# Kernel optimization log

Hardware: AMD Instinct MI355X
Metric: run time of the kernel (lower is better)

## Reference

```python
import jax, jax.numpy as jnp
import numpy as np

# dims
T, B = 64, 512
NTOK, NINP, NHID = 512, 600, 600
NB, TOPK = 6, 4          # num_blocks, update_topk
BS = NHID // NB          # block_size = 100
ATT, DK, DC = 340, 64, 32  # attention_out, input-attn key dim, comm-attn key dim


def setup_inputs() -> dict:
    key = jax.random.key(0)
    ks = jax.random.split(key, 16)
    s = 0.05
    r = lambda k, shp: (jax.random.normal(k, shp, jnp.float32) * s)
    return {
        "input": jax.random.normal(ks[0], (T, B, NTOK), jnp.float32),
        "hidden": jnp.zeros((1, B, NHID), jnp.float32),
        "masks": jnp.ones((T, B, 1), jnp.float32),
        "enc_W": r(ks[1], (NTOK, NINP)),
        "enc_b": jnp.zeros((NINP,), jnp.float32),
        "Wq": r(ks[2], (BS, DK)),
        "Wk": r(ks[3], (NINP, DK)),
        "Wv": r(ks[4], (NINP, ATT)),
        "Wx": r(ks[5], (ATT, 3 * BS)),
        "Wh": r(ks[6], (BS, 3 * BS)),
        "gru_b": jnp.zeros((3 * BS,), jnp.float32),
        "Wq2": r(ks[7], (BS, DC)),
        "Wk2": r(ks[8], (BS, DC)),
        "Wv2": r(ks[9], (BS, BS)),
        "dec_W": r(ks[10], (NHID, NTOK)),
        "dec_b": jnp.zeros((NTOK,), jnp.float32),
    }


def reference(input, hidden, masks, enc_W, enc_b, Wq, Wk, Wv, Wx, Wh, gru_b,
              Wq2, Wk2, Wv2, dec_W, dec_b):
    # encoder (continuous input path of RNNModel)
    emb = input @ enc_W + enc_b                     # [T,B,ninp]
    h0 = hidden[0]                                  # [B,nhid]
    sc1 = 1.0 / jnp.sqrt(jnp.float32(DK))
    sc2 = 1.0 / jnp.sqrt(jnp.float32(DC))

    def step(h, xt_m):
        xt, m = xt_m                                # [B,ninp], [B,1]
        h = h * m                                   # RL done-masking (h_masks)
        hb = h.reshape(B, NB, BS)                   # per-block hidden
        # --- input attention: read sources = [null, input] (num_modules_read_input=2)
        src = jnp.stack([jnp.zeros_like(xt), xt], axis=1)   # [B,2,ninp]
        kk = src @ Wk                               # [B,2,DK]
        vv = src @ Wv                               # [B,2,ATT]
        q = hb @ Wq                                 # [B,NB,DK]
        probs = jax.nn.softmax(jnp.einsum('bnd,bsd->bns', q, kk) * sc1, axis=-1)
        read = jnp.einsum('bns,bsv->bnv', probs, vv)        # [B,NB,ATT]
        # --- top-k block selection: blocks attending most to real input update
        inp_score = probs[:, :, 1]                  # [B,NB]
        _, idx = jax.lax.top_k(inp_score, TOPK)
        bmask = jax.nn.one_hot(idx, NB, dtype=h.dtype).sum(axis=1)  # [B,NB]
        # --- shared block GRU update
        xg = read @ Wx + gru_b                      # [B,NB,3*BS]
        hg = hb @ Wh                                # [B,NB,3*BS]
        r_ = jax.nn.sigmoid(xg[..., :BS] + hg[..., :BS])
        z_ = jax.nn.sigmoid(xg[..., BS:2 * BS] + hg[..., BS:2 * BS])
        n_ = jnp.tanh(xg[..., 2 * BS:] + r_ * hg[..., 2 * BS:])
        hn = (1.0 - z_) * n_ + z_ * hb              # [B,NB,BS]
        # --- communication attention among blocks (residual)
        q2, k2, v2 = hn @ Wq2, hn @ Wk2, hn @ Wv2
        p2 = jax.nn.softmax(jnp.einsum('bnd,bmd->bnm', q2, k2) * sc2, axis=-1)
        hc = hn + jnp.einsum('bnm,bmv->bnv', p2, v2)
        # --- gated write: only top-k blocks update
        mb = bmask[..., None]
        hb_new = mb * hc + (1.0 - mb) * hb
        hnew = hb_new.reshape(B, NHID)
        return hnew, (hnew, bmask)

    hT, (out, bmasks) = jax.lax.scan(step, h0, (emb, masks))
    dec = out @ dec_W + dec_b                       # [T,B,ntoken]
    return dec, hT[None], bmasks
```

## Files before the change

kernel.cpp:

```cpp
#include <hip/hip_runtime.h>
#include <hip/hip_bf16.h>
#include <stdint.h>

typedef __bf16 bf16_t;
typedef __bf16 bf16x8 __attribute__((ext_vector_type(8)));
typedef float f32x4 __attribute__((ext_vector_type(4)));

#define T_STEPS 64
#define BATCH   512
#define NTOKC   512
#define NINP    600
#define NHID    600
#define NBLK    6
#define BSZ     100
#define DK      64
#define ATTD    340
#define DC      32
#define KU_N    384
#define OUT_KP  608

#define WS_KU     0u
#define WS_OUTB   50331648u
#define WS_W1     90177536u
#define WS_B1     90963968u
#define WS_WVWX   90965504u
#define WS_DECWT  91685504u


__global__ void prep_wvwx(const float* __restrict__ Wv, const float* __restrict__ Wx,
                          float* __restrict__ WvWx) {
    int idx = blockIdx.x * 256 + threadIdx.x;
    if (idx >= NINP * 300) return;
    int i = idx / 300, c = idx % 300;
    float acc = 0.f;
    for (int a = 0; a < ATTD; a++) acc += Wv[i * ATTD + a] * Wx[a * 300 + c];
    WvWx[i * 300 + c] = acc;
}

__global__ void prep_w1(const float* __restrict__ encW, const float* __restrict__ Wk,
                        const float* __restrict__ WvWx, float* __restrict__ W1) {
    int idx = blockIdx.x * 256 + threadIdx.x;
    if (idx >= NTOKC * KU_N) return;
    int i = idx / KU_N, c = idx % KU_N;
    float acc = 0.f;
    if (c < DK) {
        for (int k = 0; k < NINP; k++) acc += encW[i * NINP + k] * Wk[k * DK + c];
    } else if (c < DK + 300) {
        int cc = c - DK;
        for (int k = 0; k < NINP; k++) acc += encW[i * NINP + k] * WvWx[k * 300 + cc];
    }
    W1[idx] = acc;
}

__global__ void prep_b1(const float* __restrict__ encB, const float* __restrict__ Wk,
                        const float* __restrict__ WvWx, float* __restrict__ b1) {
    int c = blockIdx.x * 256 + threadIdx.x;
    if (c >= KU_N) return;
    float acc = 0.f;
    if (c < DK) {
        for (int k = 0; k < NINP; k++) acc += encB[k] * Wk[k * DK + c];
    } else if (c < DK + 300) {
        int cc = c - DK;
        for (int k = 0; k < NINP; k++) acc += encB[k] * WvWx[k * 300 + cc];
    }
    b1[c] = acc;
}

__global__ void prep_decwt(const float* __restrict__ decW, bf16_t* __restrict__ decWT) {
    int idx = blockIdx.x * 256 + threadIdx.x;
    if (idx >= NTOKC * OUT_KP) return;
    int n = idx / OUT_KP, k = idx % OUT_KP;
    decWT[idx] = (k < NHID) ? (bf16_t)decW[k * NTOKC + n] : (bf16_t)0.f;
}


__global__ __launch_bounds__(256) void ku_gemm(const float* __restrict__ A,
                                               const float* __restrict__ W1,
                                               const float* __restrict__ b1,
                                               float* __restrict__ KU) {
    __shared__ float As[16][128];
    __shared__ float Bs[16][64];
    const int tid = threadIdx.x;
    const int m0 = blockIdx.x * 128, n0 = blockIdx.y * 64;
    const int ty = tid >> 4, tx = tid & 15;
    const int bk = tid >> 6, bn = tid & 63;
    float acc[8][4] = {};
    for (int k0 = 0; k0 < NTOKC; k0 += 16) {
#pragma unroll
        for (int ii = 0; ii < 2; ii++) {
            int t2 = tid + ii * 256;
            int ar = t2 >> 2, ac4 = (t2 & 3) << 2;
            float4 raw = *(const float4*)(A + (size_t)(m0 + ar) * NTOKC + k0 + ac4);
            As[ac4 + 0][ar] = raw.x;
            As[ac4 + 1][ar] = raw.y;
            As[ac4 + 2][ar] = raw.z;
            As[ac4 + 3][ar] = raw.w;
        }
#pragma unroll
        for (int i = 0; i < 4; i++) {
            int kk = bk + (i << 2);
            Bs[kk][bn] = W1[(size_t)(k0 + kk) * KU_N + n0 + bn];
        }
        __syncthreads();
#pragma unroll
        for (int kk = 0; kk < 16; kk++) {
            float4 a0 = *(const float4*)&As[kk][ty * 8];
            float4 a1 = *(const float4*)&As[kk][ty * 8 + 4];
            float4 bv = *(const float4*)&Bs[kk][tx * 4];
            float av[8] = {a0.x, a0.y, a0.z, a0.w, a1.x, a1.y, a1.z, a1.w};
            float bw[4] = {bv.x, bv.y, bv.z, bv.w};
#pragma unroll
            for (int r = 0; r < 8; r++)
#pragma unroll
                for (int c = 0; c < 4; c++) acc[r][c] += av[r] * bw[c];
        }
        __syncthreads();
    }
#pragma unroll
    for (int r = 0; r < 8; r++) {
        int m = m0 + ty * 8 + r;
#pragma unroll
        for (int c = 0; c < 4; c++) {
            int n = n0 + tx * 4 + c;
            KU[(size_t)m * KU_N + n] = acc[r][c] + b1[n];
        }
    }
}


__global__ __launch_bounds__(640) void scan_kernel(
    const float* __restrict__ hidden, const float* __restrict__ masks,
    const float* __restrict__ Wq, const float* __restrict__ Wh,
    const float* __restrict__ grub, const float* __restrict__ Wq2,
    const float* __restrict__ Wk2, const float* __restrict__ Wv2,
    const float* __restrict__ KU, bf16_t* __restrict__ outb,
    float* __restrict__ hT_out, float* __restrict__ bm_out) {
    __shared__ float h[2][NHID];
    __shared__ float u[2][300];
    __shared__ float k1s[2][DK];
    __shared__ float qb[2][NBLK][DK];
    __shared__ float p1s[2][8], bmv[2][8];
    __shared__ float hg[2][NBLK][300];
    __shared__ float qkv[2][NBLK][164];
    __shared__ float p2s[2][NBLK][8];

    const int tid = threadIdx.x;
    const int b0 = blockIdx.x * 2;

    for (int idx = tid; idx < 2 * NHID; idx += 640) {
        int b = idx / NHID, j = idx % NHID;
        h[b][j] = hidden[(size_t)(b0 + b) * NHID + j];
    }
    __syncthreads();

    for (int t = 0; t < T_STEPS; t++) {
        {
            float mv0 = masks[t * BATCH + b0];
            float mv1 = masks[t * BATCH + b0 + 1];
            for (int idx = tid; idx < 2 * NHID; idx += 640) {
                int b = idx / NHID, j = idx % NHID;
                h[b][j] *= (b ? mv1 : mv0);
            }
            for (int idx = tid; idx < 2 * 364; idx += 640) {
                int b = idx / 364, c = idx % 364;
                float v = KU[(size_t)(t * BATCH + b0 + b) * KU_N + c];
                if (c < DK) k1s[b][c] = v; else u[b][c - DK] = v;
            }
        }
        __syncthreads();
        for (int idx = tid; idx < 2 * NBLK * DK; idx += 640) {
            int b = idx / (NBLK * DK), r = idx % (NBLK * DK);
            int n = r / DK, d = r % DK;
            float acc = 0.f;
            const float* hp = &h[b][n * BSZ];
            for (int k = 0; k < BSZ; k += 4) {
                float4 h4 = *(const float4*)(hp + k);
                acc += h4.x * Wq[(k)*DK + d];
                acc += h4.y * Wq[(k + 1) * DK + d];
                acc += h4.z * Wq[(k + 2) * DK + d];
                acc += h4.w * Wq[(k + 3) * DK + d];
            }
            qb[b][n][d] = acc;
        }
        __syncthreads();
        if (tid < 2 * NBLK) {
            int b = tid / NBLK, n = tid % NBLK;
            float s = 0.f;
            for (int d = 0; d < DK; d++) s += qb[b][n][d] * k1s[b][d];
            s *= 0.125f;
            float mx = fmaxf(s, 0.f);
            float e0 = expf(0.f - mx), e1 = expf(s - mx);
            p1s[b][n] = e1 / (e0 + e1);
        }
        __syncthreads();
        if (tid < 2 * NBLK) {
            int b = tid / NBLK, n = tid % NBLK;
            float pn = p1s[b][n];
            int cnt = 0;
            for (int j = 0; j < NBLK; j++) {
                float pj = p1s[b][j];
                if (pj > pn || (pj == pn && j < n)) cnt++;
            }
            float bm = (cnt < 4) ? 1.f : 0.f;
            bmv[b][n] = bm;
            bm_out[(size_t)(t * BATCH + b0 + b) * NBLK + n] = bm;
        }
        __syncthreads();
        for (int idx = tid; idx < 600; idx += 640) {
            int b = idx / 300, c = idx % 300;
            float acc[NBLK] = {};
            for (int k = 0; k < BSZ; k += 4) {
                float w0 = Wh[(k)*300 + c];
                float w1 = Wh[(k + 1) * 300 + c];
                float w2 = Wh[(k + 2) * 300 + c];
                float w3 = Wh[(k + 3) * 300 + c];
#pragma unroll
                for (int n = 0; n < NBLK; n++) {
                    float4 h4 = *(const float4*)&h[b][n * BSZ + k];
                    acc[n] += h4.x * w0 + h4.y * w1 + h4.z * w2 + h4.w * w3;
                }
            }
#pragma unroll
            for (int n = 0; n < NBLK; n++) hg[b][n][c] = acc[n];
        }
        __syncthreads();
        for (int idx = tid; idx < 1200; idx += 640) {
            int b = idx / 600, r = idx % 600, n = r / BSZ, c = r % BSZ;
            float p1 = p1s[b][n];
            float xr = p1 * u[b][c] + grub[c];
            float xz = p1 * u[b][BSZ + c] + grub[BSZ + c];
            float xn = p1 * u[b][2 * BSZ + c] + grub[2 * BSZ + c];
            float hr = hg[b][n][c], hz = hg[b][n][BSZ + c], hnn = hg[b][n][2 * BSZ + c];
            float r_ = 1.f / (1.f + expf(-(xr + hr)));
            float z_ = 1.f / (1.f + expf(-(xz + hz)));
            float nn = tanhf(xn + r_ * hnn);
            float hold = h[b][n * BSZ + c];
            hg[b][n][c] = (1.f - z_) * nn + z_ * hold;
        }
        __syncthreads();
        for (int idx = tid; idx < 2 * 164; idx += 640) {
            int b = idx / 164, c = idx % 164;
            float acc[NBLK] = {};
            for (int k = 0; k < BSZ; k += 4) {
                float w0, w1, w2, w3;
                if (c < 32) {
                    w0 = Wq2[(k)*32 + c]; w1 = Wq2[(k + 1) * 32 + c];
                    w2 = Wq2[(k + 2) * 32 + c]; w3 = Wq2[(k + 3) * 32 + c];
                } else if (c < 64) {
                    int cc = c - 32;
                    w0 = Wk2[(k)*32 + cc]; w1 = Wk2[(k + 1) * 32 + cc];
                    w2 = Wk2[(k + 2) * 32 + cc]; w3 = Wk2[(k + 3) * 32 + cc];
                } else {
                    int cc = c - 64;
                    w0 = Wv2[(k)*100 + cc]; w1 = Wv2[(k + 1) * 100 + cc];
                    w2 = Wv2[(k + 2) * 100 + cc]; w3 = Wv2[(k + 3) * 100 + cc];
                }
#pragma unroll
                for (int n = 0; n < NBLK; n++) {
                    float4 h4 = *(const float4*)&hg[b][n][k];
                    acc[n] += h4.x * w0 + h4.y * w1 + h4.z * w2 + h4.w * w3;
                }
            }
#pragma unroll
            for (int n = 0; n < NBLK; n++) qkv[b][n][c] = acc[n];
        }
        __syncthreads();
        if (tid < 72) {
            int b = tid / 36, r = tid % 36, n = r / 6, m = r % 6;
            float e = 0.f;
            for (int d = 0; d < DC; d++) e += qkv[b][n][d] * qkv[b][m][32 + d];
            p2s[b][n][m] = e * 0.17677669529663687f;
        }
        __syncthreads();
        if (tid < 12) {
            int b = tid / 6, n = tid % 6;
            float mx = p2s[b][n][0];
            for (int m = 1; m < 6; m++) mx = fmaxf(mx, p2s[b][n][m]);
            float ev[6], sum = 0.f;
            for (int m = 0; m < 6; m++) { ev[m] = expf(p2s[b][n][m] - mx); sum += ev[m]; }
            for (int m = 0; m < 6; m++) p2s[b][n][m] = ev[m] / sum;
        }
        __syncthreads();
        for (int idx = tid; idx < 1200; idx += 640) {
            int b = idx / 600, r = idx % 600, n = r / BSZ, c = r % BSZ;
            float acc = hg[b][n][c];
#pragma unroll
            for (int m = 0; m < 6; m++) acc += p2s[b][n][m] * qkv[b][m][64 + c];
            float hold = h[b][n * BSZ + c];
            float hnew = (bmv[b][n] != 0.f) ? acc : hold;
            h[b][n * BSZ + c] = hnew;
            size_t row = (size_t)(t * BATCH + b0 + b);
            outb[row * OUT_KP + n * BSZ + c] = (bf16_t)hnew;
            if (t == T_STEPS - 1) hT_out[(size_t)(b0 + b) * NHID + n * BSZ + c] = hnew;
        }
        for (int idx = tid; idx < 2 * 8; idx += 640) {
            int b = idx / 8, c = idx % 8;
            outb[(size_t)(t * BATCH + b0 + b) * OUT_KP + NHID + c] = (bf16_t)0.f;
        }
        __syncthreads();
    }
}


__global__ __launch_bounds__(256) void dec_gemm(const bf16_t* __restrict__ Ag,
                                                const bf16_t* __restrict__ Bg,
                                                const float* __restrict__ bias,
                                                float* __restrict__ C) {
    __shared__ bf16_t As[128][32];
    __shared__ bf16_t Bs[64][32];
    const int tid = threadIdx.x;
    const int wave = tid >> 6, lane = tid & 63;
    const int m0 = blockIdx.x * 128, n0 = blockIdx.y * 64;
    f32x4 acc[2][4] = {};
    for (int k0 = 0; k0 < OUT_KP; k0 += 32) {
#pragma unroll
        for (int ii = 0; ii < 2; ii++) {
            int el = (tid + ii * 256) * 8;
            int row = el >> 5, col = el & 31;
            *(float4*)&As[row][col] = *(const float4*)(Ag + (size_t)(m0 + row) * OUT_KP + k0 + col);
        }
        {
            int el = tid * 8;
            int row = el >> 5, col = el & 31;
            *(float4*)&Bs[row][col] = *(const float4*)(Bg + (size_t)(n0 + row) * OUT_KP + k0 + col);
        }
        __syncthreads();
        const int fm = lane & 15, fq = (lane >> 4) * 8;
        bf16x8 a[2], b[4];
        a[0] = *(const bf16x8*)&As[wave * 32 + fm][fq];
        a[1] = *(const bf16x8*)&As[wave * 32 + 16 + fm][fq];
#pragma unroll
        for (int nt = 0; nt < 4; nt++) b[nt] = *(const bf16x8*)&Bs[nt * 16 + fm][fq];
#pragma unroll
        for (int mt = 0; mt < 2; mt++)
#pragma unroll
            for (int nt = 0; nt < 4; nt++)
                acc[mt][nt] = __builtin_amdgcn_mfma_f32_16x16x32_bf16(a[mt], b[nt], acc[mt][nt], 0, 0, 0);
        __syncthreads();
    }
    const int fm = lane & 15, fr = (lane >> 4) * 4;
#pragma unroll
    for (int mt = 0; mt < 2; mt++)
#pragma unroll
        for (int nt = 0; nt < 4; nt++) {
            int n = n0 + nt * 16 + fm;
            float bia = bias[n];
#pragma unroll
            for (int r = 0; r < 4; r++) {
                int m = m0 + wave * 32 + mt * 16 + fr + r;
                C[(size_t)m * NTOKC + n] = acc[mt][nt][r] + bia;
            }
        }
}


extern "C" void kernel_launch(void* const* d_in, const int* in_sizes, int n_in,
                              void* d_out, int out_size, void* d_ws, size_t ws_size,
                              hipStream_t stream) {
    const float* input  = (const float*)d_in[0];
    const float* hidden = (const float*)d_in[1];
    const float* masks  = (const float*)d_in[2];
    const float* encW   = (const float*)d_in[3];
    const float* encB   = (const float*)d_in[4];
    const float* Wq     = (const float*)d_in[5];
    const float* Wk     = (const float*)d_in[6];
    const float* Wv     = (const float*)d_in[7];
    const float* Wx     = (const float*)d_in[8];
    const float* Wh     = (const float*)d_in[9];
    const float* grub   = (const float*)d_in[10];
    const float* Wq2    = (const float*)d_in[11];
    const float* Wk2    = (const float*)d_in[12];
    const float* Wv2    = (const float*)d_in[13];
    const float* decW   = (const float*)d_in[14];
    const float* decB   = (const float*)d_in[15];

    char* ws = (char*)d_ws;
    float*  KU    = (float*)(ws + WS_KU);
    bf16_t* outb  = (bf16_t*)(ws + WS_OUTB);
    float*  W1    = (float*)(ws + WS_W1);
    float*  b1    = (float*)(ws + WS_B1);
    float*  WvWx  = (float*)(ws + WS_WVWX);
    bf16_t* decWT = (bf16_t*)(ws + WS_DECWT);

    float* out_dec = (float*)d_out;
    float* out_hT  = out_dec + 16777216;
    float* out_bm  = out_dec + 17084416;

    prep_wvwx<<<(NINP * 300 + 255) / 256, 256, 0, stream>>>(Wv, Wx, WvWx);
    prep_w1<<<(NTOKC * KU_N + 255) / 256, 256, 0, stream>>>(encW, Wk, WvWx, W1);
    prep_b1<<<2, 256, 0, stream>>>(encB, Wk, WvWx, b1);
    prep_decwt<<<(NTOKC * OUT_KP + 255) / 256, 256, 0, stream>>>(decW, decWT);
    ku_gemm<<<dim3(256, 6), 256, 0, stream>>>(input, W1, b1, KU);
    scan_kernel<<<256, 640, 0, stream>>>(hidden, masks, Wq, Wh, grub, Wq2, Wk2, Wv2,
                                         KU, outb, out_hT, out_bm);
    dec_gemm<<<dim3(256, 8), 256, 0, stream>>>(outb, decWT, decB, out_dec);
}
```

Measured before the change: 1.585 ms.

## Restructure scan kernel to one batch row per block with fused stages

The scan kernel now gives each workgroup one batch row instead of two, launching 512 blocks of 448 threads. The input-attention score is rewritten algebraically as h·(Wq·k), so the per-block Wq projection becomes a single 100-wide vector. Independent stages are merged to cut barriers: the Wh GEMV runs alongside the Wq·k product, top-k runs alongside the GRU update, and the comm softmax uses shuffles while Wv2 runs concurrently. The next step's mask and KU row are also prefetched at the end of each step, which removes the synchronization at the start of the loop.

```diff
diff --git a/kernel.cpp b/kernel.cpp
--- a/kernel.cpp
+++ b/kernel.cpp
@@ -128,174 +128,195 @@
 }
 
 
-__global__ __launch_bounds__(640) void scan_kernel(
+__global__ __launch_bounds__(448) void scan_kernel(
     const float* __restrict__ hidden, const float* __restrict__ masks,
     const float* __restrict__ Wq, const float* __restrict__ Wh,
     const float* __restrict__ grub, const float* __restrict__ Wq2,
     const float* __restrict__ Wk2, const float* __restrict__ Wv2,
     const float* __restrict__ KU, bf16_t* __restrict__ outb,
     float* __restrict__ hT_out, float* __restrict__ bm_out) {
-    __shared__ float h[2][NHID];
-    __shared__ float u[2][300];
-    __shared__ float k1s[2][DK];
-    __shared__ float qb[2][NBLK][DK];
-    __shared__ float p1s[2][8], bmv[2][8];
-    __shared__ float hg[2][NBLK][300];
-    __shared__ float qkv[2][NBLK][164];
-    __shared__ float p2s[2][NBLK][8];
+    __shared__ float h[NHID];
+    __shared__ float u[300];
+    __shared__ float k1s[DK];
+    __shared__ float wt[BSZ];
+    __shared__ float p1s[NBLK], bmv[NBLK];
+    __shared__ float hg[NBLK][300];
+    __shared__ float qkv[NBLK][164];
+    __shared__ float p2s[NBLK][6];
 
     const int tid = threadIdx.x;
-    const int b0 = blockIdx.x * 2;
-
-    for (int idx = tid; idx < 2 * NHID; idx += 640) {
-        int b = idx / NHID, j = idx % NHID;
-        h[b][j] = hidden[(size_t)(b0 + b) * NHID + j];
+    const int b = blockIdx.x;
+
+    {
+        float mv0 = masks[b];
+        for (int j = tid; j < NHID; j += 448) h[j] = hidden[(size_t)b * NHID + j] * mv0;
+        const float* kur = KU + (size_t)b * KU_N;
+        for (int c = tid; c < 364; c += 448) {
+            float v = kur[c];
+            if (c < DK) k1s[c] = v; else u[c - DK] = v;
+        }
     }
     __syncthreads();
 
     for (int t = 0; t < T_STEPS; t++) {
-        {
-            float mv0 = masks[t * BATCH + b0];
-            float mv1 = masks[t * BATCH + b0 + 1];
-            for (int idx = tid; idx < 2 * NHID; idx += 640) {
-                int b = idx / NHID, j = idx % NHID;
-                h[b][j] *= (b ? mv1 : mv0);
-            }
-            for (int idx = tid; idx < 2 * 364; idx += 640) {
-                int b = idx / 364, c = idx % 364;
-                float v = KU[(size_t)(t * BATCH + b0 + b) * KU_N + c];
-                if (c < DK) k1s[b][c] = v; else u[b][c - DK] = v;
-            }
-        }
-        __syncthreads();
-        for (int idx = tid; idx < 2 * NBLK * DK; idx += 640) {
-            int b = idx / (NBLK * DK), r = idx % (NBLK * DK);
-            int n = r / DK, d = r % DK;
+        for (int idx = tid; idx < 400; idx += 448) {
+            if (idx < 300) {
+                int c = idx;
+                float acc[NBLK] = {};
+                for (int k = 0; k < BSZ; k += 4) {
+                    float w0 = Wh[(k)*300 + c];
+                    float w1 = Wh[(k + 1) * 300 + c];
+                    float w2 = Wh[(k + 2) * 300 + c];
+                    float w3 = Wh[(k + 3) * 300 + c];
+#pragma unroll
+                    for (int n = 0; n < NBLK; n++) {
+                        float4 h4 = *(const float4*)&h[n * BSZ + k];
+                        acc[n] += h4.x * w0 + h4.y * w1 + h4.z * w2 + h4.w * w3;
+                    }
+                }
+#pragma unroll
+                for (int n = 0; n < NBLK; n++) hg[n][c] = acc[n];
+            } else {
+                int kq = idx - 300;
+                const float* wq = Wq + kq * DK;
+                float acc = 0.f;
+                for (int d = 0; d < DK; d += 4) {
+                    float4 wv = *(const float4*)(wq + d);
+                    float4 kv = *(const float4*)&k1s[d];
+                    acc += wv.x * kv.x + wv.y * kv.y + wv.z * kv.z + wv.w * kv.w;
+                }
+                wt[kq] = acc;
+            }
+        }
+        __syncthreads();
+        if (tid < 192) {
+            int n = tid >> 5, l = tid & 31;
+            float part = 0.f;
+            if (l < 25) {
+                float4 h4 = *(const float4*)&h[n * BSZ + l * 4];
+                float4 w4 = *(const float4*)&wt[l * 4];
+                part = h4.x * w4.x + h4.y * w4.y + h4.z * w4.z + h4.w * w4.w;
+            }
+            part += __shfl_down(part, 16, 32);
+            part += __shfl_down(part, 8, 32);
+            part += __shfl_down(part, 4, 32);
+            part += __shfl_down(part, 2, 32);
+            part += __shfl_down(part, 1, 32);
+            if (l == 0) {
+                float s = part * 0.125f;
+                float mx = fmaxf(s, 0.f);
+                float e0 = expf(0.f - mx), e1 = expf(s - mx);
+                p1s[n] = e1 / (e0 + e1);
+            }
+        }
+        __syncthreads();
+        for (int idx = tid; idx < 606; idx += 448) {
+            if (idx < 600) {
+                int n = idx / BSZ, c = idx % BSZ;
+                float p1 = p1s[n];
+                float xr = p1 * u[c] + grub[c];
+                float xz = p1 * u[BSZ + c] + grub[BSZ + c];
+                float xn = p1 * u[2 * BSZ + c] + grub[2 * BSZ + c];
+                float hr = hg[n][c], hz = hg[n][BSZ + c], hnn = hg[n][2 * BSZ + c];
+                float r_ = 1.f / (1.f + expf(-(xr + hr)));
+                float z_ = 1.f / (1.f + expf(-(xz + hz)));
+                float nn = tanhf(xn + r_ * hnn);
+                float hold = h[idx];
+                hg[n][c] = (1.f - z_) * nn + z_ * hold;
+            } else {
+                int n = idx - 600;
+                float pn = p1s[n];
+                int cnt = 0;
+                for (int j = 0; j < NBLK; j++) {
+                    float pj = p1s[j];
+                    if (pj > pn || (pj == pn && j < n)) cnt++;
+                }
+                float bm = (cnt < 4) ? 1.f : 0.f;
+                bmv[n] = bm;
+                bm_out[(size_t)(t * BATCH + b) * NBLK + n] = bm;
+            }
+        }
+        __syncthreads();
+        for (int idx = tid; idx < 384; idx += 448) {
+            int n = idx >> 6, c = idx & 63;
+            const float* w = (c < 32) ? (Wq2 + c) : (Wk2 + (c - 32));
             float acc = 0.f;
-            const float* hp = &h[b][n * BSZ];
             for (int k = 0; k < BSZ; k += 4) {
-                float4 h4 = *(const float4*)(hp + k);
-                acc += h4.x * Wq[(k)*DK + d];
-                acc += h4.y * Wq[(k + 1) * DK + d];
-                acc += h4.z * Wq[(k + 2) * DK + d];
-                acc += h4.w * Wq[(k + 3) * DK + d];
-            }
-            qb[b][n][d] = acc;
-        }
-        __syncthreads();
-        if (tid < 2 * NBLK) {
-            int b = tid / NBLK, n = tid % NBLK;
-            float s = 0.f;
-            for (int d = 0; d < DK; d++) s += qb[b][n][d] * k1s[b][d];
-            s *= 0.125f;
-            float mx = fmaxf(s, 0.f);
-            float e0 = expf(0.f - mx), e1 = expf(s - mx);
-            p1s[b][n] = e1 / (e0 + e1);
-        }
-        __syncthreads();
-        if (tid < 2 * NBLK) {
-            int b = tid / NBLK, n = tid % NBLK;
-            float pn = p1s[b][n];
-            int cnt = 0;
-            for (int j = 0; j < NBLK; j++) {
-                float pj = p1s[b][j];
-                if (pj > pn || (pj == pn && j < n)) cnt++;
-            }
-            float bm = (cnt < 4) ? 1.f : 0.f;
-            bmv[b][n] = bm;
-            bm_out[(size_t)(t * BATCH + b0 + b) * NBLK + n] = bm;
-        }
-        __syncthreads();
-        for (int idx = tid; idx < 600; idx += 640) {
-            int b = idx / 300, c = idx % 300;
-            float acc[NBLK] = {};
-            for (int k = 0; k < BSZ; k += 4) {
-                float w0 = Wh[(k)*300 + c];
-                float w1 = Wh[(k + 1) * 300 + c];
-                float w2 = Wh[(k + 2) * 300 + c];
-                float w3 = Wh[(k + 3) * 300 + c];
-#pragma unroll
-                for (int n = 0; n < NBLK; n++) {
-                    float4 h4 = *(const float4*)&h[b][n * BSZ + k];
-                    acc[n] += h4.x * w0 + h4.y * w1 + h4.z * w2 + h4.w * w3;
+                float4 h4 = *(const float4*)&hg[n][k];
+                acc += h4.x * w[(k)*32] + h4.y * w[(k + 1) * 32] +
+                       h4.z * w[(k + 2) * 32] + h4.w * w[(k + 3) * 32];
+            }
+            qkv[n][c] = acc;
+        }
+        __syncthreads();
+        if (tid < 64) {
+            if (tid < 36) {
+                int n = tid / 6;
+                int m = tid - n * 6;
+                float e = 0.f;
+                for (int d = 0; d < DC; d += 4) {
+                    float4 q4 = *(const float4*)&qkv[n][d];
+                    float4 k4 = *(const float4*)&qkv[m][32 + d];
+                    e += q4.x * k4.x + q4.y * k4.y + q4.z * k4.z + q4.w * k4.w;
                 }
-            }
-#pragma unroll
-            for (int n = 0; n < NBLK; n++) hg[b][n][c] = acc[n];
-        }
-        __syncthreads();
-        for (int idx = tid; idx < 1200; idx += 640) {
-            int b = idx / 600, r = idx % 600, n = r / BSZ, c = r % BSZ;
-            float p1 = p1s[b][n];
-            float xr = p1 * u[b][c] + grub[c];
-            float xz = p1 * u[b][BSZ + c] + grub[BSZ + c];
-            float xn = p1 * u[b][2 * BSZ + c] + grub[2 * BSZ + c];
-            float hr = hg[b][n][c], hz = hg[b][n][BSZ + c], hnn = hg[b][n][2 * BSZ + c];
-            float r_ = 1.f / (1.f + expf(-(xr + hr)));
-            float z_ = 1.f / (1.f + expf(-(xz + hz)));
-            float nn = tanhf(xn + r_ * hnn);
-            float hold = h[b][n * BSZ + c];
-            hg[b][n][c] = (1.f - z_) * nn + z_ * hold;
-        }
-        __syncthreads();
-        for (int idx = tid; idx < 2 * 164; idx += 640) {
-            int b = idx / 164, c = idx % 164;
-            float acc[NBLK] = {};
-            for (int k = 0; k < BSZ; k += 4) {
-                float w0, w1, w2, w3;
-                if (c < 32) {
-                    w0 = Wq2[(k)*32 + c]; w1 = Wq2[(k + 1) * 32 + c];
-                    w2 = Wq2[(k + 2) * 32 + c]; w3 = Wq2[(k + 3) * 32 + c];
-                } else if (c < 64) {
-                    int cc = c - 32;
-                    w0 = Wk2[(k)*32 + cc]; w1 = Wk2[(k + 1) * 32 + cc];
-                    w2 = Wk2[(k + 2) * 32 + cc]; w3 = Wk2[(k + 3) * 32 + cc];
-                } else {
-                    int cc = c - 64;
-                    w0 = Wv2[(k)*100 + cc]; w1 = Wv2[(k + 1) * 100 + cc];
-                    w2 = Wv2[(k + 2) * 100 + cc]; w3 = Wv2[(k + 3) * 100 + cc];
+                e *= 0.17677669529663687f;
+                float ev[6];
+#pragma unroll
+                for (int j = 0; j < 6; j++) ev[j] = __shfl(e, n * 6 + j, 64);
+                float mx = ev[0];
+#pragma unroll
+                for (int j = 1; j < 6; j++) mx = fmaxf(mx, ev[j]);
+                float sum = 0.f;
+#pragma unroll
+                for (int j = 0; j < 6; j++) sum += expf(ev[j] - mx);
+                p2s[n][m] = expf(e - mx) / sum;
+            }
+        } else {
+            int idx = tid - 64;
+            if (idx < 200) {
+                int nb = (idx / 100) * 3, c = idx % 100;
+                float a0 = 0.f, a1 = 0.f, a2 = 0.f;
+                for (int k = 0; k < BSZ; k += 4) {
+                    float w0 = Wv2[(k)*100 + c];
+                    float w1 = Wv2[(k + 1) * 100 + c];
+                    float w2 = Wv2[(k + 2) * 100 + c];
+                    float w3 = Wv2[(k + 3) * 100 + c];
+                    float4 h0 = *(const float4*)&hg[nb][k];
+                    float4 h1 = *(const float4*)&hg[nb + 1][k];
+                    float4 h2 = *(const float4*)&hg[nb + 2][k];
+                    a0 += h0.x * w0 + h0.y * w1 + h0.z * w2 + h0.w * w3;
+                    a1 += h1.x * w0 + h1.y * w1 + h1.z * w2 + h1.w * w3;
+                    a2 += h2.x * w0 + h2.y * w1 + h2.z * w2 + h2.w * w3;
                 }
-#pragma unroll
-                for (int n = 0; n < NBLK; n++) {
-                    float4 h4 = *(const float4*)&hg[b][n][k];
-                    acc[n] += h4.x * w0 + h4.y * w1 + h4.z * w2 + h4.w * w3;
-                }
-            }
-#pragma unroll
-            for (int n = 0; n < NBLK; n++) qkv[b][n][c] = acc[n];
-        }
-        __syncthreads();
-        if (tid < 72) {
-            int b = tid / 36, r = tid % 36, n = r / 6, m = r % 6;
-            float e = 0.f;
-            for (int d = 0; d < DC; d++) e += qkv[b][n][d] * qkv[b][m][32 + d];
-            p2s[b][n][m] = e * 0.17677669529663687f;
-        }
-        __syncthreads();
-        if (tid < 12) {
-            int b = tid / 6, n = tid % 6;
-            float mx = p2s[b][n][0];
-            for (int m = 1; m < 6; m++) mx = fmaxf(mx, p2s[b][n][m]);
-            float ev[6], sum = 0.f;
-            for (int m = 0; m < 6; m++) { ev[m] = expf(p2s[b][n][m] - mx); sum += ev[m]; }
-            for (int m = 0; m < 6; m++) p2s[b][n][m] = ev[m] / sum;
-        }
-        __syncthreads();
-        for (int idx = tid; idx < 1200; idx += 640) {
-            int b = idx / 600, r = idx % 600, n = r / BSZ, c = r % BSZ;
-            float acc = hg[b][n][c];
-#pragma unroll
-            for (int m = 0; m < 6; m++) acc += p2s[b][n][m] * qkv[b][m][64 + c];
-            float hold = h[b][n * BSZ + c];
-            float hnew = (bmv[b][n] != 0.f) ? acc : hold;
-            h[b][n * BSZ + c] = hnew;
-            size_t row = (size_t)(t * BATCH + b0 + b);
-            outb[row * OUT_KP + n * BSZ + c] = (bf16_t)hnew;
-            if (t == T_STEPS - 1) hT_out[(size_t)(b0 + b) * NHID + n * BSZ + c] = hnew;
-        }
-        for (int idx = tid; idx < 2 * 8; idx += 640) {
-            int b = idx / 8, c = idx % 8;
-            outb[(size_t)(t * BATCH + b0 + b) * OUT_KP + NHID + c] = (bf16_t)0.f;
+                qkv[nb][64 + c] = a0;
+                qkv[nb + 1][64 + c] = a1;
+                qkv[nb + 2][64 + c] = a2;
+            }
+        }
+        __syncthreads();
+        float mv_next = (t < T_STEPS - 1) ? masks[(t + 1) * BATCH + b] : 1.f;
+        size_t row = (size_t)(t * BATCH + b);
+        for (int idx = tid; idx < 608; idx += 448) {
+            if (idx < 600) {
+                int n = idx / BSZ, c = idx % BSZ;
+                float acc = hg[n][c];
+#pragma unroll
+                for (int m = 0; m < 6; m++) acc += p2s[n][m] * qkv[m][64 + c];
+                float hold = h[idx];
+                float hnew = (bmv[n] != 0.f) ? acc : hold;
+                h[idx] = hnew * mv_next;
+                outb[row * OUT_KP + idx] = (bf16_t)hnew;
+                if (t == T_STEPS - 1) hT_out[(size_t)b * NHID + idx] = hnew;
+            } else {
+                outb[row * OUT_KP + NHID + (idx - 600)] = (bf16_t)0.f;
+            }
+        }
+        if (t < T_STEPS - 1) {
+            const float* kur = KU + (size_t)((t + 1) * BATCH + b) * KU_N;
+            for (int c = tid; c < 364; c += 448) {
+                float v = kur[c];
+                if (c < DK) k1s[c] = v; else u[c - DK] = v;
+            }
         }
         __syncthreads();
     }
@@ -326,16 +347,16 @@
         }
         __syncthreads();
         const int fm = lane & 15, fq = (lane >> 4) * 8;
-        bf16x8 a[2], b[4];
+        bf16x8 a[2], bfr[4];
         a[0] = *(const bf16x8*)&As[wave * 32 + fm][fq];
         a[1] = *(const bf16x8*)&As[wave * 32 + 16 + fm][fq];
 #pragma unroll
-        for (int nt = 0; nt < 4; nt++) b[nt] = *(const bf16x8*)&Bs[nt * 16 + fm][fq];
+        for (int nt = 0; nt < 4; nt++) bfr[nt] = *(const bf16x8*)&Bs[nt * 16 + fm][fq];
 #pragma unroll
         for (int mt = 0; mt < 2; mt++)
 #pragma unroll
             for (int nt = 0; nt < 4; nt++)
-                acc[mt][nt] = __builtin_amdgcn_mfma_f32_16x16x32_bf16(a[mt], b[nt], acc[mt][nt], 0, 0, 0);
+                acc[mt][nt] = __builtin_amdgcn_mfma_f32_16x16x32_bf16(a[mt], bfr[nt], acc[mt][nt], 0, 0, 0);
         __syncthreads();
     }
     const int fm = lane & 15, fr = (lane >> 4) * 4;
@@ -391,7 +412,7 @@
     prep_b1<<<2, 256, 0, stream>>>(encB, Wk, WvWx, b1);
     prep_decwt<<<(NTOKC * OUT_KP + 255) / 256, 256, 0, stream>>>(decW, decWT);
     ku_gemm<<<dim3(256, 6), 256, 0, stream>>>(input, W1, b1, KU);
-    scan_kernel<<<256, 640, 0, stream>>>(hidden, masks, Wq, Wh, grub, Wq2, Wk2, Wv2,
+    scan_kernel<<<512, 448, 0, stream>>>(hidden, masks, Wq, Wh, grub, Wq2, Wk2, Wv2,
                                          KU, outb, out_hT, out_bm);
     dec_gemm<<<dim3(256, 8), 256, 0, stream>>>(outb, decWT, decB, out_dec);
 }
```

Result: slower. 5.505 ms (+247.4%).

## Cut barriers in scan step by fusing attention stages and prefetching next inputs

Applied to the files above, without the earlier changes.

Restructures the per-timestep scan loop to reduce the number of __syncthreads per step. The input-attention query projection and score reduction are fused into one wave-per-block pass using shuffle reductions. The Wh matvec now shares a phase with it, and top-k selection moves into the GRU phase. Comm-attention scores and softmax are done with shuffles, running concurrently with the Wv2 projection on other threads. The next step's mask and KU loads fold into the final write phase, adding more index logic and ordering subtleties in exchange.

```diff
diff --git a/kernel.cpp b/kernel.cpp
--- a/kernel.cpp
+++ b/kernel.cpp
@@ -138,74 +138,57 @@
     __shared__ float h[2][NHID];
     __shared__ float u[2][300];
     __shared__ float k1s[2][DK];
-    __shared__ float qb[2][NBLK][DK];
-    __shared__ float p1s[2][8], bmv[2][8];
+    __shared__ float p1s[2][NBLK], bmv[2][NBLK];
     __shared__ float hg[2][NBLK][300];
     __shared__ float qkv[2][NBLK][164];
-    __shared__ float p2s[2][NBLK][8];
+    __shared__ float p2s[2][NBLK][6];
 
     const int tid = threadIdx.x;
     const int b0 = blockIdx.x * 2;
 
-    for (int idx = tid; idx < 2 * NHID; idx += 640) {
-        int b = idx / NHID, j = idx % NHID;
-        h[b][j] = hidden[(size_t)(b0 + b) * NHID + j];
+    {
+        float mv0 = masks[b0];
+        float mv1 = masks[b0 + 1];
+        for (int idx = tid; idx < 2 * NHID; idx += 640) {
+            int b = idx / NHID, j = idx % NHID;
+            h[b][j] = hidden[(size_t)(b0 + b) * NHID + j] * (b ? mv1 : mv0);
+        }
+        for (int idx = tid; idx < 2 * 364; idx += 640) {
+            int b = idx / 364, c = idx % 364;
+            float v = KU[(size_t)(b0 + b) * KU_N + c];
+            if (c < DK) k1s[b][c] = v; else u[b][c - DK] = v;
+        }
     }
     __syncthreads();
 
     for (int t = 0; t < T_STEPS; t++) {
         {
-            float mv0 = masks[t * BATCH + b0];
-            float mv1 = masks[t * BATCH + b0 + 1];
-            for (int idx = tid; idx < 2 * NHID; idx += 640) {
-                int b = idx / NHID, j = idx % NHID;
-                h[b][j] *= (b ? mv1 : mv0);
-            }
-            for (int idx = tid; idx < 2 * 364; idx += 640) {
-                int b = idx / 364, c = idx % 364;
-                float v = KU[(size_t)(t * BATCH + b0 + b) * KU_N + c];
-                if (c < DK) k1s[b][c] = v; else u[b][c - DK] = v;
-            }
-        }
-        __syncthreads();
-        for (int idx = tid; idx < 2 * NBLK * DK; idx += 640) {
-            int b = idx / (NBLK * DK), r = idx % (NBLK * DK);
-            int n = r / DK, d = r % DK;
-            float acc = 0.f;
-            const float* hp = &h[b][n * BSZ];
-            for (int k = 0; k < BSZ; k += 4) {
-                float4 h4 = *(const float4*)(hp + k);
-                acc += h4.x * Wq[(k)*DK + d];
-                acc += h4.y * Wq[(k + 1) * DK + d];
-                acc += h4.z * Wq[(k + 2) * DK + d];
-                acc += h4.w * Wq[(k + 3) * DK + d];
-            }
-            qb[b][n][d] = acc;
-        }
-        __syncthreads();
-        if (tid < 2 * NBLK) {
-            int b = tid / NBLK, n = tid % NBLK;
-            float s = 0.f;
-            for (int d = 0; d < DK; d++) s += qb[b][n][d] * k1s[b][d];
-            s *= 0.125f;
-            float mx = fmaxf(s, 0.f);
-            float e0 = expf(0.f - mx), e1 = expf(s - mx);
-            p1s[b][n] = e1 / (e0 + e1);
-        }
-        __syncthreads();
-        if (tid < 2 * NBLK) {
-            int b = tid / NBLK, n = tid % NBLK;
-            float pn = p1s[b][n];
-            int cnt = 0;
-            for (int j = 0; j < NBLK; j++) {
-                float pj = p1s[b][j];
-                if (pj > pn || (pj == pn && j < n)) cnt++;
-            }
-            float bm = (cnt < 4) ? 1.f : 0.f;
-            bmv[b][n] = bm;
-            bm_out[(size_t)(t * BATCH + b0 + b) * NBLK + n] = bm;
-        }
-        __syncthreads();
+            int w = tid >> 6, l = tid & 63;
+            for (int j = w; j < 12; j += 10) {
+                int b = j / 6, n = j % 6;
+                const float* hp = &h[b][n * BSZ];
+                float a0 = 0.f, a1 = 0.f, a2 = 0.f, a3 = 0.f;
+                for (int k = 0; k < BSZ; k += 4) {
+                    a0 += hp[k + 0] * Wq[(k + 0) * DK + l];
+                    a1 += hp[k + 1] * Wq[(k + 1) * DK + l];
+                    a2 += hp[k + 2] * Wq[(k + 2) * DK + l];
+                    a3 += hp[k + 3] * Wq[(k + 3) * DK + l];
+                }
+                float part = ((a0 + a1) + (a2 + a3)) * k1s[b][l];
+                part += __shfl_down(part, 32);
+                part += __shfl_down(part, 16);
+                part += __shfl_down(part, 8);
+                part += __shfl_down(part, 4);
+                part += __shfl_down(part, 2);
+                part += __shfl_down(part, 1);
+                if (l == 0) {
+                    float s = part * 0.125f;
+                    float mx = fmaxf(s, 0.f);
+                    float e0 = expf(0.f - mx), e1 = expf(s - mx);
+                    p1s[b][n] = e1 / (e0 + e1);
+                }
+            }
+        }
         for (int idx = tid; idx < 600; idx += 640) {
             int b = idx / 300, c = idx % 300;
             float acc[NBLK] = {};
@@ -234,68 +217,104 @@
             float r_ = 1.f / (1.f + expf(-(xr + hr)));
             float z_ = 1.f / (1.f + expf(-(xz + hz)));
             float nn = tanhf(xn + r_ * hnn);
-            float hold = h[b][n * BSZ + c];
+            float hold = h[b][r];
             hg[b][n][c] = (1.f - z_) * nn + z_ * hold;
         }
-        __syncthreads();
-        for (int idx = tid; idx < 2 * 164; idx += 640) {
-            int b = idx / 164, c = idx % 164;
-            float acc[NBLK] = {};
-            for (int k = 0; k < BSZ; k += 4) {
-                float w0, w1, w2, w3;
-                if (c < 32) {
-                    w0 = Wq2[(k)*32 + c]; w1 = Wq2[(k + 1) * 32 + c];
-                    w2 = Wq2[(k + 2) * 32 + c]; w3 = Wq2[(k + 3) * 32 + c];
-                } else if (c < 64) {
-                    int cc = c - 32;
-                    w0 = Wk2[(k)*32 + cc]; w1 = Wk2[(k + 1) * 32 + cc];
-                    w2 = Wk2[(k + 2) * 32 + cc]; w3 = Wk2[(k + 3) * 32 + cc];
-                } else {
-                    int cc = c - 64;
-                    w0 = Wv2[(k)*100 + cc]; w1 = Wv2[(k + 1) * 100 + cc];
-                    w2 = Wv2[(k + 2) * 100 + cc]; w3 = Wv2[(k + 3) * 100 + cc];
-                }
-#pragma unroll
-                for (int n = 0; n < NBLK; n++) {
-                    float4 h4 = *(const float4*)&hg[b][n][k];
-                    acc[n] += h4.x * w0 + h4.y * w1 + h4.z * w2 + h4.w * w3;
-                }
-            }
-#pragma unroll
-            for (int n = 0; n < NBLK; n++) qkv[b][n][c] = acc[n];
-        }
-        __syncthreads();
-        if (tid < 72) {
-            int b = tid / 36, r = tid % 36, n = r / 6, m = r % 6;
-            float e = 0.f;
-            for (int d = 0; d < DC; d++) e += qkv[b][n][d] * qkv[b][m][32 + d];
-            p2s[b][n][m] = e * 0.17677669529663687f;
-        }
-        __syncthreads();
         if (tid < 12) {
             int b = tid / 6, n = tid % 6;
-            float mx = p2s[b][n][0];
-            for (int m = 1; m < 6; m++) mx = fmaxf(mx, p2s[b][n][m]);
-            float ev[6], sum = 0.f;
-            for (int m = 0; m < 6; m++) { ev[m] = expf(p2s[b][n][m] - mx); sum += ev[m]; }
-            for (int m = 0; m < 6; m++) p2s[b][n][m] = ev[m] / sum;
-        }
-        __syncthreads();
-        for (int idx = tid; idx < 1200; idx += 640) {
-            int b = idx / 600, r = idx % 600, n = r / BSZ, c = r % BSZ;
-            float acc = hg[b][n][c];
-#pragma unroll
-            for (int m = 0; m < 6; m++) acc += p2s[b][n][m] * qkv[b][m][64 + c];
-            float hold = h[b][n * BSZ + c];
-            float hnew = (bmv[b][n] != 0.f) ? acc : hold;
-            h[b][n * BSZ + c] = hnew;
-            size_t row = (size_t)(t * BATCH + b0 + b);
-            outb[row * OUT_KP + n * BSZ + c] = (bf16_t)hnew;
-            if (t == T_STEPS - 1) hT_out[(size_t)(b0 + b) * NHID + n * BSZ + c] = hnew;
-        }
-        for (int idx = tid; idx < 2 * 8; idx += 640) {
-            int b = idx / 8, c = idx % 8;
-            outb[(size_t)(t * BATCH + b0 + b) * OUT_KP + NHID + c] = (bf16_t)0.f;
+            float pn = p1s[b][n];
+            int cnt = 0;
+            for (int j = 0; j < NBLK; j++) {
+                float pj = p1s[b][j];
+                if (pj > pn || (pj == pn && j < n)) cnt++;
+            }
+            float bm = (cnt < 4) ? 1.f : 0.f;
+            bmv[b][n] = bm;
+            bm_out[(size_t)(t * BATCH + b0 + b) * NBLK + n] = bm;
+        }
+        __syncthreads();
+        for (int idx = tid; idx < 768; idx += 640) {
+            int b = idx / 384, r = idx % 384, n = r >> 6, c = r & 63;
+            const float* w = (c < 32) ? (Wq2 + c) : (Wk2 + (c - 32));
+            float acc = 0.f;
+            for (int k = 0; k < BSZ; k += 4) {
+                float4 h4 = *(const float4*)&hg[b][n][k];
+                acc += h4.x * w[(k)*32] + h4.y * w[(k + 1) * 32] +
+                       h4.z * w[(k + 2) * 32] + h4.w * w[(k + 3) * 32];
+            }
+            qkv[b][n][c] = acc;
+        }
+        __syncthreads();
+        if (tid < 128) {
+            int b = tid >> 6, l = tid & 63;
+            if (l < 36) {
+                int n = l / 6, m = l % 6;
+                float e = 0.f;
+                for (int d = 0; d < DC; d += 4) {
+                    float4 q4 = *(const float4*)&qkv[b][n][d];
+                    float4 k4 = *(const float4*)&qkv[b][m][32 + d];
+                    e += q4.x * k4.x + q4.y * k4.y + q4.z * k4.z + q4.w * k4.w;
+                }
+                e *= 0.17677669529663687f;
+                float ev[6];
+#pragma unroll
+                for (int j = 0; j < 6; j++) ev[j] = __shfl(e, n * 6 + j, 64);
+                float mx = ev[0];
+#pragma unroll
+                for (int j = 1; j < 6; j++) mx = fmaxf(mx, ev[j]);
+                float sum = 0.f;
+#pragma unroll
+                for (int j = 0; j < 6; j++) sum += expf(ev[j] - mx);
+                p2s[b][n][m] = expf(e - mx) / sum;
+            }
+        } else if (tid < 528) {
+            int idx = tid - 128;
+            int b = idx / 200, g = (idx % 200) / 100, c = idx % 100;
+            int nb = g * 3;
+            float a0 = 0.f, a1 = 0.f, a2 = 0.f;
+            for (int k = 0; k < BSZ; k += 4) {
+                float w0 = Wv2[(k)*100 + c];
+                float w1 = Wv2[(k + 1) * 100 + c];
+                float w2 = Wv2[(k + 2) * 100 + c];
+                float w3 = Wv2[(k + 3) * 100 + c];
+                float4 h0 = *(const float4*)&hg[b][nb][k];
+                float4 h1 = *(const float4*)&hg[b][nb + 1][k];
+                float4 h2 = *(const float4*)&hg[b][nb + 2][k];
+                a0 += h0.x * w0 + h0.y * w1 + h0.z * w2 + h0.w * w3;
+                a1 += h1.x * w0 + h1.y * w1 + h1.z * w2 + h1.w * w3;
+                a2 += h2.x * w0 + h2.y * w1 + h2.z * w2 + h2.w * w3;
+            }
+            qkv[b][nb][64 + c] = a0;
+            qkv[b][nb + 1][64 + c] = a1;
+            qkv[b][nb + 2][64 + c] = a2;
+        }
+        __syncthreads();
+        {
+            float mvn0 = (t < T_STEPS - 1) ? masks[(t + 1) * BATCH + b0] : 1.f;
+            float mvn1 = (t < T_STEPS - 1) ? masks[(t + 1) * BATCH + b0 + 1] : 1.f;
+            for (int idx = tid; idx < 1200; idx += 640) {
+                int b = idx / 600, r = idx % 600, n = r / BSZ, c = r % BSZ;
+                float acc = hg[b][n][c];
+#pragma unroll
+                for (int m = 0; m < 6; m++) acc += p2s[b][n][m] * qkv[b][m][64 + c];
+                float hold = h[b][r];
+                float hnew = (bmv[b][n] != 0.f) ? acc : hold;
+                h[b][r] = hnew * (b ? mvn1 : mvn0);
+                size_t row = (size_t)(t * BATCH + b0 + b);
+                outb[row * OUT_KP + r] = (bf16_t)hnew;
+                if (t == T_STEPS - 1) hT_out[(size_t)(b0 + b) * NHID + r] = hnew;
+            }
+            if (tid < 16) {
+                int b = tid >> 3;
+                outb[(size_t)(t * BATCH + b0 + b) * OUT_KP + NHID + (tid & 7)] = (bf16_t)0.f;
+            }
+            if (t < T_STEPS - 1) {
+                for (int idx = tid; idx < 728; idx += 640) {
+                    int b = idx / 364, c = idx % 364;
+                    float v = KU[(size_t)((t + 1) * BATCH + b0 + b) * KU_N + c];
+                    if (c < DK) k1s[b][c] = v; else u[b][c - DK] = v;
+                }
+            }
         }
         __syncthreads();
     }
@@ -326,16 +345,16 @@
         }
         __syncthreads();
         const int fm = lane & 15, fq = (lane >> 4) * 8;
-        bf16x8 a[2], b[4];
+        bf16x8 a[2], bfr[4];
         a[0] = *(const bf16x8*)&As[wave * 32 + fm][fq];
         a[1] = *(const bf16x8*)&As[wave * 32 + 16 + fm][fq];
 #pragma unroll
-        for (int nt = 0; nt < 4; nt++) b[nt] = *(const bf16x8*)&Bs[nt * 16 + fm][fq];
+        for (int nt = 0; nt < 4; nt++) bfr[nt] = *(const bf16x8*)&Bs[nt * 16 + fm][fq];
 #pragma unroll
         for (int mt = 0; mt < 2; mt++)
 #pragma unroll
             for (int nt = 0; nt < 4; nt++)
-                acc[mt][nt] = __builtin_amdgcn_mfma_f32_16x16x32_bf16(a[mt], b[nt], acc[mt][nt], 0, 0, 0);
+                acc[mt][nt] = __builtin_amdgcn_mfma_f32_16x16x32_bf16(a[mt], bfr[nt], acc[mt][nt], 0, 0, 0);
         __syncthreads();
     }
     const int fm = lane & 15, fr = (lane >> 4) * 4;
```

After: 4.172 ms. +163.3%, slower.
